# Kernel tuning notes

Measured on AMD Instinct MI355X. Metric: run time of the kernel, lower is better.

Reference implementation:

```python
import jax, jax.numpy as jnp
import numpy as np

B, NNZ = 2048, 8
CAT_V, HVEC_V = 10000, 50000
SYN, SEM = 128, 256
HIDDEN, OUT = 1024, 10000


def setup_inputs() -> dict:
    key = jax.random.key(0)
    ks = jax.random.split(key, 12)
    d_onehot = jax.nn.one_hot(jax.random.randint(ks[0], (B,), 0, 7), 7, dtype=jnp.float32)
    cat_b_ix = jax.random.randint(ks[1], (B,), 0, CAT_V)
    hvb_ix = jax.random.randint(ks[2], (B, NNZ), 0, HVEC_V)
    hvf_ix = jax.random.randint(ks[3], (B, NNZ), 0, HVEC_V)
    hvb_top = jax.random.normal(ks[4], (B, SEM), dtype=jnp.float32)
    hvf_top = jax.random.normal(ks[5], (B, SEM), dtype=jnp.float32)
    cat_embeds = jax.random.normal(ks[6], (CAT_V, SYN), dtype=jnp.float32) * 0.02
    hvec_embeds = jax.random.normal(ks[7], (HVEC_V, SEM), dtype=jnp.float32) * 0.02
    in_dim = 7 + SYN + 2 * SEM
    W1 = jax.random.normal(ks[8], (HIDDEN, in_dim), dtype=jnp.float32) / np.sqrt(in_dim)
    b1 = jnp.zeros((HIDDEN,), dtype=jnp.float32)
    W2 = jax.random.normal(ks[9], (OUT, HIDDEN), dtype=jnp.float32) / np.sqrt(HIDDEN)
    b2 = jnp.zeros((OUT,), dtype=jnp.float32)
    return {"d_onehot": d_onehot, "cat_b_ix": cat_b_ix, "hvb_ix": hvb_ix,
            "hvf_ix": hvf_ix, "hvb_top": hvb_top, "hvf_top": hvf_top,
            "cat_embeds": cat_embeds, "hvec_embeds": hvec_embeds,
            "W1": W1, "b1": b1, "W2": W2, "b2": b2}


def _multi_hot(ix, vocab):
    # set-to-1 semantics: duplicates within a row still yield 1 (matches torch loop)
    rows = jnp.arange(ix.shape[0])[:, None]
    return jnp.zeros((ix.shape[0], vocab), dtype=jnp.float32).at[rows, ix].set(1.0)


def reference(d_onehot, cat_b_ix, hvb_ix, hvf_ix, hvb_top, hvf_top,
              cat_embeds, hvec_embeds, W1, b1, W2, b2):
    cat_b_embed = cat_embeds[cat_b_ix]                      # (B, SYN)
    hvb_mat = _multi_hot(hvb_ix, hvec_embeds.shape[0])      # (B, HVEC_V)
    hvf_mat = _multi_hot(hvf_ix, hvec_embeds.shape[0])
    hvb_embed = hvb_mat @ hvec_embeds + hvb_top             # (B, SEM)
    hvf_embed = hvf_mat @ hvec_embeds + hvf_top
    x = jnp.concatenate([cat_b_embed, hvb_embed, hvf_embed, d_onehot], axis=1)
    x = jax.nn.relu(x @ W1.T + b1)
    x = x @ W2.T + b2
    return jax.nn.log_softmax(x, axis=1)
```

## Files before the change

kernel.cpp:

```cpp
#include <hip/hip_runtime.h>

#define B_      2048
#define SYN     128
#define SEM     256
#define IN_DIM  647
#define K1      704
#define HIDDEN  1024
#define OUT_N   10000
#define NNZ     8

typedef __bf16 bf16x8 __attribute__((ext_vector_type(8)));
typedef float  f32x4  __attribute__((ext_vector_type(4)));
typedef __attribute__((address_space(3))) const unsigned short* lds_cp;

__device__ __forceinline__ unsigned short f2b(float v) {
    __bf16 b = (__bf16)v;
    return __builtin_bit_cast(unsigned short, b);
}

#define NB_W1 2816
#define NB_W2 5000
__global__ __launch_bounds__(256) void prep(
    const float* __restrict__ W1,  unsigned short* __restrict__ W1b,
    const float* __restrict__ W2,  unsigned short* __restrict__ W2b,
    const float* __restrict__ d_onehot,
    const int*   __restrict__ cat_ix,
    const int*   __restrict__ hvb_ix,
    const int*   __restrict__ hvf_ix,
    const float* __restrict__ hvb_top,
    const float* __restrict__ hvf_top,
    const float* __restrict__ cat_embeds,
    const float* __restrict__ hvec_embeds,
    unsigned short* __restrict__ xb)
{
    const int bb = blockIdx.x, t = threadIdx.x;
    if (bb < NB_W1) {
        int idx = bb * 256 + t;
        int r = idx / K1, c = idx - r * K1;
        W1b[idx] = f2b(c < IN_DIM ? W1[r * IN_DIM + c] : 0.f);
        return;
    }
    if (bb < NB_W1 + NB_W2) {
        size_t i = (size_t)(bb - NB_W1) * 256 + t;
        const float4* src = (const float4*)(W2 + i * 8);
        float4 a = src[0], b = src[1];
        ushort u[8] = { f2b(a.x), f2b(a.y), f2b(a.z), f2b(a.w),
                        f2b(b.x), f2b(b.y), f2b(b.z), f2b(b.w) };
        *(uint4*)(W2b + i * 8) = *(const uint4*)u;
        return;
    }
    const int b = bb - (NB_W1 + NB_W2);
    unsigned short* xrow = xb + (size_t)b * K1;
    if (t < SYN) {
        int c = cat_ix[b];
        xrow[t] = f2b(cat_embeds[(size_t)c * SYN + t]);
    }
    {
        int ix[NNZ];
        #pragma unroll
        for (int j = 0; j < NNZ; ++j) ix[j] = hvb_ix[b * NNZ + j];
        float s = hvb_top[(size_t)b * SEM + t];
        #pragma unroll
        for (int j = 0; j < NNZ; ++j) {
            bool dup = false;
            for (int k2 = 0; k2 < j; ++k2) dup = dup || (ix[j] == ix[k2]);
            if (!dup) s += hvec_embeds[(size_t)ix[j] * SEM + t];
        }
        xrow[SYN + t] = f2b(s);
    }
    {
        int ix[NNZ];
        #pragma unroll
        for (int j = 0; j < NNZ; ++j) ix[j] = hvf_ix[b * NNZ + j];
        float s = hvf_top[(size_t)b * SEM + t];
        #pragma unroll
        for (int j = 0; j < NNZ; ++j) {
            bool dup = false;
            for (int k2 = 0; k2 < j; ++k2) dup = dup || (ix[j] == ix[k2]);
            if (!dup) s += hvec_embeds[(size_t)ix[j] * SEM + t];
        }
        xrow[SYN + SEM + t] = f2b(s);
    }
    if (t < 7)       xrow[640 + t] = f2b(d_onehot[b * 7 + t]);
    else if (t < 64) xrow[640 + t] = 0;
}

template<int NI, int MODE>
__global__ __launch_bounds__(256) void gemm_rt(
    const unsigned short* __restrict__ A,
    const unsigned short* __restrict__ Bm,
    const float* __restrict__ bias,
    void* __restrict__ outp,
    int K, int nt, int ncols, int nbm1, int nm)
{
    constexpr int BN    = 32 * NI;
    constexpr int NB_CH = NI / 2;
    __shared__ __align__(16) unsigned short lds_a[4][128 * 32];
    __shared__ __align__(16) unsigned short lds_b[4][BN * 32];

    const int tid = threadIdx.x;
    const int wv = tid >> 6, ln = tid & 63;
    const int wr = wv >> 1, wc = wv & 1;
    const int lr = ln & 15, lh = ln >> 4;

    const int g   = gridDim.x;
    const int nw  = (blockIdx.x & 7) * (g >> 3) + (blockIdx.x >> 3);
    const int mt  = nw % nm, ntile = nw / nm;
    const int m0  = mt * 128, n0 = ntile * BN;

    const unsigned short* srcA[2];
    const unsigned short* srcB[NB_CH];
    #pragma unroll
    for (int i = 0; i < 2; ++i) {
        int c = tid + i * 256;
        int row = c >> 2, colL = (((c & 3) ^ ((c >> 3) & 3)) << 3);
        srcA[i] = A + (size_t)(m0 + row) * K + colL;
    }
    #pragma unroll
    for (int j = 0; j < NB_CH; ++j) {
        int c = tid + j * 256;
        int row = c >> 2, colL = (((c & 3) ^ ((c >> 3) & 3)) << 3);
        int gr = n0 + row; if (gr > nbm1) gr = nbm1;
        srcB[j] = Bm + (size_t)gr * K + colL;
    }

    auto stage = [&](int buf, int kt) {
        #pragma unroll
        for (int i = 0; i < 2; ++i)
            __builtin_amdgcn_global_load_lds(
                (__attribute__((address_space(1))) const void*)(srcA[i] + kt),
                (__attribute__((address_space(3))) void*)&lds_a[buf][(tid + i * 256) * 8], 16, 0, 0);
        #pragma unroll
        for (int j = 0; j < NB_CH; ++j)
            __builtin_amdgcn_global_load_lds(
                (__attribute__((address_space(1))) const void*)(srcB[j] + kt),
                (__attribute__((address_space(3))) void*)&lds_b[buf][(tid + j * 256) * 8], 16, 0, 0);
    };

    int a_off[4], b_off[NI];
    #pragma unroll
    for (int mi = 0; mi < 4; ++mi) {
        int row = wr * 64 + mi * 16 + lr;
        a_off[mi] = (row * 64 + lh * 16) ^ (((row >> 1) & 3) << 4);
    }
    #pragma unroll
    for (int ni = 0; ni < NI; ++ni) {
        int row = wc * 16 * NI + ni * 16 + lr;
        b_off[ni] = (row * 64 + lh * 16) ^ (((row >> 1) & 3) << 4);
    }

    f32x4 acc[4][NI];
    {
        f32x4 z = {0.f, 0.f, 0.f, 0.f};
        #pragma unroll
        for (int i = 0; i < 4; ++i)
            #pragma unroll
            for (int j = 0; j < NI; ++j) acc[i][j] = z;
    }

    auto frag_read = [&](bf16x8 (&af)[4], bf16x8 (&bfv)[NI], int buf) {
        lds_cp pa = (lds_cp)&lds_a[buf][0];
        lds_cp pb = (lds_cp)&lds_b[buf][0];
        #pragma unroll
        for (int mi = 0; mi < 4; ++mi) {
            unsigned ad = (unsigned)(unsigned long long)pa + a_off[mi];
            asm volatile("ds_read_b128 %0, %1" : "=v"(af[mi]) : "v"(ad));
        }
        #pragma unroll
        for (int ni = 0; ni < NI; ++ni) {
            unsigned ad = (unsigned)(unsigned long long)pb + b_off[ni];
            asm volatile("ds_read_b128 %0, %1" : "=v"(bfv[ni]) : "v"(ad));
        }
    };
    auto do_mfma = [&](bf16x8 (&af)[4], bf16x8 (&bfv)[NI]) {
        #pragma unroll
        for (int mi = 0; mi < 4; ++mi)
            #pragma unroll
            for (int ni = 0; ni < NI; ++ni)
                acc[mi][ni] = __builtin_amdgcn_mfma_f32_16x16x32_bf16(af[mi], bfv[ni], acc[mi][ni], 0, 0, 0);
    };
    auto do_part = [&](bf16x8 (&rA)[4], bf16x8 (&rB)[NI],
                       bf16x8 (&mA)[4], bf16x8 (&mB)[NI], int p) {
        frag_read(rA, rB, (p + 1) & 3);
        int tp = p + 3; if (tp > nt - 1) tp = nt - 1;
        stage((p + 3) & 3, tp * 32);
        if constexpr (NI == 4) asm volatile("s_waitcnt lgkmcnt(8)" ::: "memory");
        else                   asm volatile("s_waitcnt lgkmcnt(6)" ::: "memory");
        __builtin_amdgcn_sched_barrier(0);
        __builtin_amdgcn_s_setprio(1);
        do_mfma(mA, mB);
        __builtin_amdgcn_s_setprio(0);
        if constexpr (NI == 4) asm volatile("s_waitcnt vmcnt(4)" ::: "memory");
        else                   asm volatile("s_waitcnt vmcnt(3)" ::: "memory");
        __builtin_amdgcn_s_barrier();
    };

    stage(0, 0);
    stage(1, 32);
    stage(2, 64);
    if constexpr (NI == 4) asm volatile("s_waitcnt vmcnt(4)" ::: "memory");
    else                   asm volatile("s_waitcnt vmcnt(3)" ::: "memory");
    __builtin_amdgcn_s_barrier();

    bf16x8 afX[4], bfX[NI], afY[4], bfY[NI];
    frag_read(afX, bfX, 0);

    for (int t = 0; t < nt; t += 2) {
        do_part(afY, bfY, afX, bfX, t);
        do_part(afX, bfX, afY, bfY, t + 1);
    }

    #pragma unroll
    for (int mi = 0; mi < 4; ++mi) {
        int row = m0 + wr * 64 + mi * 16 + lh * 4;
        #pragma unroll
        for (int ni = 0; ni < NI; ++ni) {
            int col = n0 + wc * 16 * NI + ni * 16 + lr;
            if (col < ncols) {
                float bb = bias[col];
                if (MODE == 0) {
                    unsigned short* H = (unsigned short*)outp;
                    #pragma unroll
                    for (int r = 0; r < 4; ++r)
                        H[(size_t)(row + r) * ncols + col] = f2b(fmaxf(acc[mi][ni][r] + bb, 0.f));
                } else {
                    float* O = (float*)outp;
                    #pragma unroll
                    for (int r = 0; r < 4; ++r)
                        O[(size_t)(row + r) * ncols + col] = acc[mi][ni][r] + bb;
                }
            }
        }
    }
}

__global__ __launch_bounds__(512, 2) void gemm2_m(
    const unsigned short* __restrict__ A,
    const unsigned short* __restrict__ Bm,
    const float* __restrict__ bias,
    unsigned short* __restrict__ H)
{
    __shared__ __align__(16) unsigned short lA[4][8192];
    __shared__ __align__(16) unsigned short lB[4][10240];
    const int tid = threadIdx.x;
    const int wv = tid >> 6, ln = tid & 63;
    const int wr = wv >> 2, wc = wv & 3;
    const int lr = ln & 15, lh = ln >> 4;

    const int nw = (blockIdx.x & 7) * 32 + (blockIdx.x >> 3);
    const int m0 = (nw & 7) * 256;
    const int n0 = (nw >> 3) * 320;

    const unsigned short* srcA[2];
    const unsigned short* srcB[2];
    const unsigned short* srcB2;
    #pragma unroll
    for (int j = 0; j < 2; ++j) {
        int c = j * 512 + tid;
        int row = c >> 2, colL = (((c & 3) ^ ((c >> 3) & 3)) << 3);
        srcA[j] = A + (size_t)(m0 + row) * HIDDEN + colL;
        int gr = n0 + row; if (gr > OUT_N - 1) gr = OUT_N - 1;
        srcB[j] = Bm + (size_t)gr * HIDDEN + colL;
    }
    const int c2 = 1024 + (wv & 3) * 64 + ln;
    {
        int row = c2 >> 2, colL = (((c2 & 3) ^ ((c2 >> 3) & 3)) << 3);
        int gr = n0 + row; if (gr > OUT_N - 1) gr = OUT_N - 1;
        srcB2 = Bm + (size_t)gr * HIDDEN + colL;
    }

    auto stageA = [&](int slot, int kt) {
        #pragma unroll
        for (int j = 0; j < 2; ++j)
            __builtin_amdgcn_global_load_lds(
                (__attribute__((address_space(1))) const void*)(srcA[j] + kt),
                (__attribute__((address_space(3))) void*)&lA[slot][(j * 512 + tid) * 8], 16, 0, 0);
    };
    auto stageB = [&](int slot, int kt) {
        #pragma unroll
        for (int j = 0; j < 2; ++j)
            __builtin_amdgcn_global_load_lds(
                (__attribute__((address_space(1))) const void*)(srcB[j] + kt),
                (__attribute__((address_space(3))) void*)&lB[slot][(j * 512 + tid) * 8], 16, 0, 0);
        __builtin_amdgcn_global_load_lds(
            (__attribute__((address_space(1))) const void*)(srcB2 + kt),
            (__attribute__((address_space(3))) void*)&lB[slot][c2 * 8], 16, 0, 0);
    };

    int a_off[8], b_off[5];
    #pragma unroll
    for (int mi = 0; mi < 8; ++mi) {
        int row = wr * 128 + mi * 16 + lr;
        a_off[mi] = (row * 64 + lh * 16) ^ (((row >> 1) & 3) << 4);
    }
    #pragma unroll
    for (int ni = 0; ni < 5; ++ni) {
        int row = wc * 80 + ni * 16 + lr;
        b_off[ni] = (row * 64 + lh * 16) ^ (((row >> 1) & 3) << 4);
    }

    f32x4 acc[8][5];
    {
        f32x4 z = {0.f, 0.f, 0.f, 0.f};
        #pragma unroll
        for (int i = 0; i < 8; ++i)
            #pragma unroll
            for (int j = 0; j < 5; ++j) acc[i][j] = z;
    }

    stageA(0, 0);  stageB(0, 0);
    stageA(1, 32); stageB(1, 32);
    stageA(2, 64); stageB(2, 64);
    asm volatile("s_waitcnt vmcnt(10)" ::: "memory");
    __builtin_amdgcn_s_barrier();

    for (int t = 0; t < 32; ++t) {
        const int slot = t & 3;
        const int wsl  = (t + 3) & 3;
        int tp = t + 3; if (tp > 31) tp = 31;
        lds_cp pA = (lds_cp)&lA[slot][0];
        lds_cp pB = (lds_cp)&lB[slot][0];
        bf16x8 af[8], bfv[5];

        #pragma unroll
        for (int ni = 0; ni < 5; ++ni) {
            unsigned ad = (unsigned)(unsigned long long)pB + b_off[ni];
            asm volatile("ds_read_b128 %0, %1" : "=v"(bfv[ni]) : "v"(ad));
        }
        #pragma unroll
        for (int mi = 0; mi < 8; ++mi) {
            unsigned ad = (unsigned)(unsigned long long)pA + a_off[mi];
            asm volatile("ds_read_b128 %0, %1" : "=v"(af[mi]) : "v"(ad));
        }
        stageA(wsl, tp * 32);
        stageB(wsl, tp * 32);

        asm volatile("s_waitcnt lgkmcnt(4)" ::: "memory");
        __builtin_amdgcn_sched_barrier(0);
        __builtin_amdgcn_s_setprio(1);
        #pragma unroll
        for (int mi = 0; mi < 4; ++mi)
            #pragma unroll
            for (int ni = 0; ni < 5; ++ni)
                acc[mi][ni] = __builtin_amdgcn_mfma_f32_16x16x32_bf16(af[mi], bfv[ni], acc[mi][ni], 0, 0, 0);
        __builtin_amdgcn_s_setprio(0);

        asm volatile("s_waitcnt lgkmcnt(0)" ::: "memory");
        __builtin_amdgcn_sched_barrier(0);
        __builtin_amdgcn_s_setprio(1);
        #pragma unroll
        for (int mi = 0; mi < 4; ++mi)
            #pragma unroll
            for (int ni = 0; ni < 5; ++ni)
                acc[4 + mi][ni] = __builtin_amdgcn_mfma_f32_16x16x32_bf16(af[4 + mi], bfv[ni], acc[4 + mi][ni], 0, 0, 0);
        __builtin_amdgcn_s_setprio(0);

        asm volatile("s_waitcnt vmcnt(10)" ::: "memory");
        __builtin_amdgcn_s_barrier();
    }

    #pragma unroll
    for (int mi = 0; mi < 8; ++mi) {
        int row = m0 + wr * 128 + mi * 16 + lh * 4;
        #pragma unroll
        for (int ni = 0; ni < 5; ++ni) {
            int col = n0 + wc * 80 + ni * 16 + lr;
            if (col < OUT_N) {
                float bb = bias[col];
                #pragma unroll
                for (int r = 0; r < 4; ++r)
                    H[(size_t)(row + r) * OUT_N + col] = f2b(acc[mi][ni][r] + bb);
            }
        }
    }
}

__global__ __launch_bounds__(256) void lsm_b(const unsigned short* __restrict__ lg,
                                             float* __restrict__ out) {
    __shared__ __align__(16) uint4 rowbuf[1250];
    __shared__ float redm[4], reds[4];
    __shared__ float s_lz;
    const int t = threadIdx.x, wv = t >> 6, ln = t & 63;
    const unsigned short* l = lg + (size_t)blockIdx.x * OUT_N;
    float* o = out + (size_t)blockIdx.x * OUT_N;

    float m = -3.4e38f, s = 0.f;
    for (int i = t; i < 1250; i += 256) {
        uint4 v = ((const uint4*)l)[i];
        rowbuf[i] = v;
        unsigned w[4] = {v.x, v.y, v.z, v.w};
        float f[8];
        #pragma unroll
        for (int j = 0; j < 4; ++j) {
            f[2*j]   = __builtin_bit_cast(float, w[j] << 16);
            f[2*j+1] = __builtin_bit_cast(float, w[j] & 0xffff0000u);
        }
        float cm = fmaxf(fmaxf(fmaxf(f[0], f[1]), fmaxf(f[2], f[3])),
                         fmaxf(fmaxf(f[4], f[5]), fmaxf(f[6], f[7])));
        if (cm > m) { s *= __expf(m - cm); m = cm; }
        #pragma unroll
        for (int j = 0; j < 8; ++j) s += __expf(f[j] - m);
    }
    #pragma unroll
    for (int off = 32; off > 0; off >>= 1) {
        float om = __shfl_xor(m, off, 64);
        float os = __shfl_xor(s, off, 64);
        float nm = fmaxf(m, om);
        s = s * __expf(m - nm) + os * __expf(om - nm);
        m = nm;
    }
    if (ln == 0) { redm[wv] = m; reds[wv] = s; }
    __syncthreads();
    if (t == 0) {
        float gm = fmaxf(fmaxf(redm[0], redm[1]), fmaxf(redm[2], redm[3]));
        float gs = reds[0] * __expf(redm[0] - gm) + reds[1] * __expf(redm[1] - gm)
                 + reds[2] * __expf(redm[2] - gm) + reds[3] * __expf(redm[3] - gm);
        s_lz = gm + logf(gs);
    }
    __syncthreads();
    const float lz = s_lz;

    for (int i = t; i < 1250; i += 256) {
        uint4 v = rowbuf[i];
        unsigned w[4] = {v.x, v.y, v.z, v.w};
        float4 o0, o1;
        o0.x = __builtin_bit_cast(float, w[0] << 16)          - lz;
        o0.y = __builtin_bit_cast(float, w[0] & 0xffff0000u)  - lz;
        o0.z = __builtin_bit_cast(float, w[1] << 16)          - lz;
        o0.w = __builtin_bit_cast(float, w[1] & 0xffff0000u)  - lz;
        o1.x = __builtin_bit_cast(float, w[2] << 16)          - lz;
        o1.y = __builtin_bit_cast(float, w[2] & 0xffff0000u)  - lz;
        o1.z = __builtin_bit_cast(float, w[3] << 16)          - lz;
        o1.w = __builtin_bit_cast(float, w[3] & 0xffff0000u)  - lz;
        ((float4*)o)[2 * i]     = o0;
        ((float4*)o)[2 * i + 1] = o1;
    }
}

__global__ __launch_bounds__(256) void lsm_f(float* __restrict__ out) {
    __shared__ __align__(16) float rowbuf[OUT_N];
    __shared__ float red[8];
    const int t = threadIdx.x, wv = t >> 6, ln = t & 63;
    float* o = out + (size_t)blockIdx.x * OUT_N;

    float mx = -3.4e38f;
    for (int i = t; i < OUT_N / 4; i += 256) {
        float4 v = ((const float4*)o)[i];
        rowbuf[i*4] = v.x; rowbuf[i*4+1] = v.y; rowbuf[i*4+2] = v.z; rowbuf[i*4+3] = v.w;
        mx = fmaxf(fmaxf(mx, fmaxf(v.x, v.y)), fmaxf(v.z, v.w));
    }
    #pragma unroll
    for (int off = 32; off > 0; off >>= 1) mx = fmaxf(mx, __shfl_xor(mx, off, 64));
    if (ln == 0) red[wv] = mx;
    __syncthreads();
    float m4 = fmaxf(fmaxf(red[0], red[1]), fmaxf(red[2], red[3]));

    float s = 0.f;
    for (int i = t; i < OUT_N; i += 256) s += __expf(rowbuf[i] - m4);
    #pragma unroll
    for (int off = 32; off > 0; off >>= 1) s += __shfl_xor(s, off, 64);
    if (ln == 0) red[4 + wv] = s;
    __syncthreads();
    float lz = m4 + logf(red[4] + red[5] + red[6] + red[7]);

    for (int i = t; i < OUT_N / 4; i += 256) {
        float4 v = { rowbuf[i*4] - lz, rowbuf[i*4+1] - lz,
                     rowbuf[i*4+2] - lz, rowbuf[i*4+3] - lz };
        ((float4*)o)[i] = v;
    }
}

extern "C" void kernel_launch(void* const* d_in, const int* in_sizes, int n_in,
                              void* d_out, int out_size, void* d_ws, size_t ws_size,
                              hipStream_t stream) {
    const float* d_onehot    = (const float*)d_in[0];
    const int*   cat_ix      = (const int*)  d_in[1];
    const int*   hvb_ix      = (const int*)  d_in[2];
    const int*   hvf_ix      = (const int*)  d_in[3];
    const float* hvb_top     = (const float*)d_in[4];
    const float* hvf_top     = (const float*)d_in[5];
    const float* cat_embeds  = (const float*)d_in[6];
    const float* hvec_embeds = (const float*)d_in[7];
    const float* W1          = (const float*)d_in[8];
    const float* b1          = (const float*)d_in[9];
    const float* W2          = (const float*)d_in[10];
    const float* b2          = (const float*)d_in[11];
    float* out = (float*)d_out;

    unsigned short* xb  = (unsigned short*)d_ws;
    unsigned short* W1b = xb  + (size_t)B_ * K1;
    unsigned short* hB  = W1b + (size_t)HIDDEN * K1;
    unsigned short* W2b = hB  + (size_t)B_ * HIDDEN;
    unsigned short* lg  = W2b + (size_t)OUT_N * HIDDEN;
    const size_t need = ((size_t)B_*K1 + (size_t)HIDDEN*K1 + (size_t)B_*HIDDEN
                         + (size_t)OUT_N*HIDDEN + (size_t)B_*OUT_N) * 2;
    const bool bf16_logits = (ws_size >= need);

    prep<<<dim3(NB_W1 + NB_W2 + B_), dim3(256), 0, stream>>>(
        W1, W1b, W2, W2b, d_onehot, cat_ix, hvb_ix, hvf_ix,
        hvb_top, hvf_top, cat_embeds, hvec_embeds, xb);
    gemm_rt<2, 0><<<dim3(256), dim3(256), 0, stream>>>(
        xb, W1b, b1, (void*)hB, K1, K1 / 32, HIDDEN, HIDDEN - 1, 16);
    if (bf16_logits) {
        gemm2_m<<<dim3(256), dim3(512), 0, stream>>>(hB, W2b, b2, lg);
        lsm_b<<<dim3(B_), dim3(256), 0, stream>>>(lg, out);
    } else {
        gemm_rt<4, 2><<<dim3(16 * 79), dim3(256), 0, stream>>>(
            hB, W2b, b2, (void*)out, HIDDEN, HIDDEN / 32, OUT_N, OUT_N - 1, 16);
        lsm_f<<<dim3(B_), dim3(256), 0, stream>>>(out);
    }
}
```

Measured before the change: 98.96 us.

## Overlap W2 bf16 conversion with first GEMM in a combined kernel

Measured after the change: 97.06 us. Within noise of the previous version (-1.9%).

```diff
diff --git a/kernel.cpp b/kernel.cpp
--- a/kernel.cpp
+++ b/kernel.cpp
@@ -20,9 +20,8 @@
 
 #define NB_W1 2816
 #define NB_W2 5000
-__global__ __launch_bounds__(256) void prep(
+__global__ __launch_bounds__(256) void prep_light(
     const float* __restrict__ W1,  unsigned short* __restrict__ W1b,
-    const float* __restrict__ W2,  unsigned short* __restrict__ W2b,
     const float* __restrict__ d_onehot,
     const int*   __restrict__ cat_ix,
     const int*   __restrict__ hvb_ix,
@@ -40,8 +39,52 @@
         W1b[idx] = f2b(c < IN_DIM ? W1[r * IN_DIM + c] : 0.f);
         return;
     }
-    if (bb < NB_W1 + NB_W2) {
-        size_t i = (size_t)(bb - NB_W1) * 256 + t;
+    const int b = bb - NB_W1;
+    unsigned short* xrow = xb + (size_t)b * K1;
+    if (t < SYN) {
+        int c = cat_ix[b];
+        xrow[t] = f2b(cat_embeds[(size_t)c * SYN + t]);
+    }
+    {
+        int ix[NNZ];
+        #pragma unroll
+        for (int j = 0; j < NNZ; ++j) ix[j] = hvb_ix[b * NNZ + j];
+        float s = hvb_top[(size_t)b * SEM + t];
+        #pragma unroll
+        for (int j = 0; j < NNZ; ++j) {
+            bool dup = false;
+            for (int k2 = 0; k2 < j; ++k2) dup = dup || (ix[j] == ix[k2]);
+            if (!dup) s += hvec_embeds[(size_t)ix[j] * SEM + t];
+        }
+        xrow[SYN + t] = f2b(s);
+    }
+    {
+        int ix[NNZ];
+        #pragma unroll
+        for (int j = 0; j < NNZ; ++j) ix[j] = hvf_ix[b * NNZ + j];
+        float s = hvf_top[(size_t)b * SEM + t];
+        #pragma unroll
+        for (int j = 0; j < NNZ; ++j) {
+            bool dup = false;
+            for (int k2 = 0; k2 < j; ++k2) dup = dup || (ix[j] == ix[k2]);
+            if (!dup) s += hvec_embeds[(size_t)ix[j] * SEM + t];
+        }
+        xrow[SYN + SEM + t] = f2b(s);
+    }
+    if (t < 7)       xrow[640 + t] = f2b(d_onehot[b * 7 + t]);
+    else if (t < 64) xrow[640 + t] = 0;
+}
+
+__global__ __launch_bounds__(256) void mid(
+    const unsigned short* __restrict__ A,
+    const unsigned short* __restrict__ Bm,
+    const float* __restrict__ bias,
+    unsigned short* __restrict__ H,
+    const float* __restrict__ W2,
+    unsigned short* __restrict__ W2b)
+{
+    if (blockIdx.x >= 256) {
+        size_t i = (size_t)(blockIdx.x - 256) * 256 + threadIdx.x;
         const float4* src = (const float4*)(W2 + i * 8);
         float4 a = src[0], b = src[1];
         ushort u[8] = { f2b(a.x), f2b(a.y), f2b(a.z), f2b(a.w),
@@ -49,40 +92,129 @@
         *(uint4*)(W2b + i * 8) = *(const uint4*)u;
         return;
     }
-    const int b = bb - (NB_W1 + NB_W2);
-    unsigned short* xrow = xb + (size_t)b * K1;
-    if (t < SYN) {
-        int c = cat_ix[b];
-        xrow[t] = f2b(cat_embeds[(size_t)c * SYN + t]);
+
+    constexpr int NI = 2, nt = K1 / 32, K = K1, ncols = HIDDEN, nbm1 = HIDDEN - 1;
+    __shared__ __align__(16) unsigned short lds_a[4][128 * 32];
+    __shared__ __align__(16) unsigned short lds_b[4][64 * 32];
+
+    const int tid = threadIdx.x;
+    const int wv = tid >> 6, ln = tid & 63;
+    const int wr = wv >> 1, wc = wv & 1;
+    const int lr = ln & 15, lh = ln >> 4;
+
+    const int vbid = blockIdx.x;
+    const int nw  = (vbid & 7) * 32 + (vbid >> 3);
+    const int mt  = nw % 16, ntile = nw / 16;
+    const int m0  = mt * 128, n0 = ntile * 64;
+
+    const unsigned short* srcA[2];
+    const unsigned short* srcB[1];
+    #pragma unroll
+    for (int i = 0; i < 2; ++i) {
+        int c = tid + i * 256;
+        int row = c >> 2, colL = (((c & 3) ^ ((c >> 3) & 3)) << 3);
+        srcA[i] = A + (size_t)(m0 + row) * K + colL;
     }
     {
-        int ix[NNZ];
-        #pragma unroll
-        for (int j = 0; j < NNZ; ++j) ix[j] = hvb_ix[b * NNZ + j];
-        float s = hvb_top[(size_t)b * SEM + t];
-        #pragma unroll
-        for (int j = 0; j < NNZ; ++j) {
-            bool dup = false;
-            for (int k2 = 0; k2 < j; ++k2) dup = dup || (ix[j] == ix[k2]);
-            if (!dup) s += hvec_embeds[(size_t)ix[j] * SEM + t];
-        }
-        xrow[SYN + t] = f2b(s);
-    }
+        int c = tid;
+        int row = c >> 2, colL = (((c & 3) ^ ((c >> 3) & 3)) << 3);
+        int gr = n0 + row; if (gr > nbm1) gr = nbm1;
+        srcB[0] = Bm + (size_t)gr * K + colL;
+    }
+
+    auto stage = [&](int buf, int kt) {
+        #pragma unroll
+        for (int i = 0; i < 2; ++i)
+            __builtin_amdgcn_global_load_lds(
+                (__attribute__((address_space(1))) const void*)(srcA[i] + kt),
+                (__attribute__((address_space(3))) void*)&lds_a[buf][(tid + i * 256) * 8], 16, 0, 0);
+        __builtin_amdgcn_global_load_lds(
+            (__attribute__((address_space(1))) const void*)(srcB[0] + kt),
+            (__attribute__((address_space(3))) void*)&lds_b[buf][tid * 8], 16, 0, 0);
+    };
+
+    int a_off[4], b_off[NI];
+    #pragma unroll
+    for (int mi = 0; mi < 4; ++mi) {
+        int row = wr * 64 + mi * 16 + lr;
+        a_off[mi] = (row * 64 + lh * 16) ^ (((row >> 1) & 3) << 4);
+    }
+    #pragma unroll
+    for (int ni = 0; ni < NI; ++ni) {
+        int row = wc * 32 + ni * 16 + lr;
+        b_off[ni] = (row * 64 + lh * 16) ^ (((row >> 1) & 3) << 4);
+    }
+
+    f32x4 acc[4][NI];
     {
-        int ix[NNZ];
-        #pragma unroll
-        for (int j = 0; j < NNZ; ++j) ix[j] = hvf_ix[b * NNZ + j];
-        float s = hvf_top[(size_t)b * SEM + t];
-        #pragma unroll
-        for (int j = 0; j < NNZ; ++j) {
-            bool dup = false;
-            for (int k2 = 0; k2 < j; ++k2) dup = dup || (ix[j] == ix[k2]);
-            if (!dup) s += hvec_embeds[(size_t)ix[j] * SEM + t];
-        }
-        xrow[SYN + SEM + t] = f2b(s);
-    }
-    if (t < 7)       xrow[640 + t] = f2b(d_onehot[b * 7 + t]);
-    else if (t < 64) xrow[640 + t] = 0;
+        f32x4 z = {0.f, 0.f, 0.f, 0.f};
+        #pragma unroll
+        for (int i = 0; i < 4; ++i)
+            #pragma unroll
+            for (int j = 0; j < NI; ++j) acc[i][j] = z;
+    }
+
+    auto frag_read = [&](bf16x8 (&af)[4], bf16x8 (&bfv)[NI], int buf) {
+        lds_cp pa = (lds_cp)&lds_a[buf][0];
+        lds_cp pb = (lds_cp)&lds_b[buf][0];
+        #pragma unroll
+        for (int mi = 0; mi < 4; ++mi) {
+            unsigned ad = (unsigned)(unsigned long long)pa + a_off[mi];
+            asm volatile("ds_read_b128 %0, %1" : "=v"(af[mi]) : "v"(ad));
+        }
+        #pragma unroll
+        for (int ni = 0; ni < NI; ++ni) {
+            unsigned ad = (unsigned)(unsigned long long)pb + b_off[ni];
+            asm volatile("ds_read_b128 %0, %1" : "=v"(bfv[ni]) : "v"(ad));
+        }
+    };
+    auto do_mfma = [&](bf16x8 (&af)[4], bf16x8 (&bfv)[NI]) {
+        #pragma unroll
+        for (int mi = 0; mi < 4; ++mi)
+            #pragma unroll
+            for (int ni = 0; ni < NI; ++ni)
+                acc[mi][ni] = __builtin_amdgcn_mfma_f32_16x16x32_bf16(af[mi], bfv[ni], acc[mi][ni], 0, 0, 0);
+    };
+    auto do_part = [&](bf16x8 (&rA)[4], bf16x8 (&rB)[NI],
+                       bf16x8 (&mA)[4], bf16x8 (&mB)[NI], int p) {
+        frag_read(rA, rB, (p + 1) & 3);
+        int tp = p + 3; if (tp > nt - 1) tp = nt - 1;
+        stage((p + 3) & 3, tp * 32);
+        asm volatile("s_waitcnt lgkmcnt(6)" ::: "memory");
+        __builtin_amdgcn_sched_barrier(0);
+        __builtin_amdgcn_s_setprio(1);
+        do_mfma(mA, mB);
+        __builtin_amdgcn_s_setprio(0);
+        asm volatile("s_waitcnt vmcnt(3)" ::: "memory");
+        __builtin_amdgcn_s_barrier();
+    };
+
+    stage(0, 0);
+    stage(1, 32);
+    stage(2, 64);
+    asm volatile("s_waitcnt vmcnt(3)" ::: "memory");
+    __builtin_amdgcn_s_barrier();
+
+    bf16x8 afX[4], bfX[NI], afY[4], bfY[NI];
+    frag_read(afX, bfX, 0);
+
+    for (int t = 0; t < nt; t += 2) {
+        do_part(afY, bfY, afX, bfX, t);
+        do_part(afX, bfX, afY, bfY, t + 1);
+    }
+
+    #pragma unroll
+    for (int mi = 0; mi < 4; ++mi) {
+        int row = m0 + wr * 64 + mi * 16 + lh * 4;
+        #pragma unroll
+        for (int ni = 0; ni < NI; ++ni) {
+            int col = n0 + wc * 32 + ni * 16 + lr;
+            float bb = bias[col];
+            #pragma unroll
+            for (int r = 0; r < 4; ++r)
+                H[(size_t)(row + r) * ncols + col] = f2b(fmaxf(acc[mi][ni][r] + bb, 0.f));
+        }
+    }
 }
 
 template<int NI, int MODE>
@@ -496,11 +628,10 @@
                          + (size_t)OUT_N*HIDDEN + (size_t)B_*OUT_N) * 2;
     const bool bf16_logits = (ws_size >= need);
 
-    prep<<<dim3(NB_W1 + NB_W2 + B_), dim3(256), 0, stream>>>(
-        W1, W1b, W2, W2b, d_onehot, cat_ix, hvb_ix, hvf_ix,
+    prep_light<<<dim3(NB_W1 + B_), dim3(256), 0, stream>>>(
+        W1, W1b, d_onehot, cat_ix, hvb_ix, hvf_ix,
         hvb_top, hvf_top, cat_embeds, hvec_embeds, xb);
-    gemm_rt<2, 0><<<dim3(256), dim3(256), 0, stream>>>(
-        xb, W1b, b1, (void*)hB, K1, K1 / 32, HIDDEN, HIDDEN - 1, 16);
+    mid<<<dim3(256 + NB_W2), dim3(256), 0, stream>>>(xb, W1b, b1, hB, W2, W2b);
     if (bf16_logits) {
         gemm2_m<<<dim3(256), dim3(512), 0, stream>>>(hB, W2b, b2, lg);
         lsm_b<<<dim3(B_), dim3(256), 0, stream>>>(lg, out);
```
